# Kernel tuning notes

Measured on AMD Instinct MI355X. Metric: run time of the kernel, lower is better.

## Reference

```python
import jax, jax.numpy as jnp
import numpy as np

D, H, E, HID, TOPK = 1024, 16, 8, 2048, 2
B, L = 2, 2048

def setup_inputs() -> dict:
    key = jax.random.key(0)
    ks = jax.random.split(key, 12)
    s = 0.02
    return {
        "x": jax.random.normal(ks[0], (B, L, D), jnp.float32),
        "mask": jnp.zeros((B, L), dtype=bool),  # key_padding_mask: True = ignore
        "ln1_g": jnp.ones((D,), jnp.float32), "ln1_b": jnp.zeros((D,), jnp.float32),
        "Wqkv": jax.random.normal(ks[1], (3 * D, D), jnp.float32) * s,
        "bqkv": jnp.zeros((3 * D,), jnp.float32),
        "Wo": jax.random.normal(ks[2], (D, D), jnp.float32) * s,
        "bo": jnp.zeros((D,), jnp.float32),
        "ln2_g": jnp.ones((D,), jnp.float32), "ln2_b": jnp.zeros((D,), jnp.float32),
        "Wg": jax.random.normal(ks[3], (D, E), jnp.float32) * s,
        "bg": jnp.zeros((E,), jnp.float32),
        "W1": jax.random.normal(ks[4], (E, D, HID), jnp.float32) * s,
        "b1": jnp.zeros((E, HID), jnp.float32),
        "W2": jax.random.normal(ks[5], (E, HID, D), jnp.float32) * s,
        "b2": jnp.zeros((E, D), jnp.float32),
    }

def _layernorm(x, g, b, eps=1e-5):
    mu = x.mean(-1, keepdims=True)
    var = ((x - mu) ** 2).mean(-1, keepdims=True)
    return (x - mu) * jax.lax.rsqrt(var + eps) * g + b

def reference(x, mask, ln1_g, ln1_b, Wqkv, bqkv, Wo, bo, ln2_g, ln2_b, Wg, bg, W1, b1, W2, b2):
    b, l, d = x.shape
    dh = d // H
    # ---- pre-norm self-attention ----
    residual = x
    xn = _layernorm(x, ln1_g, ln1_b)
    qkv = xn @ Wqkv.T + bqkv                      # [B,L,3D]
    q, k, v = jnp.split(qkv, 3, axis=-1)
    q = q.reshape(b, l, H, dh).transpose(0, 2, 1, 3)  # bhld
    k = k.reshape(b, l, H, dh).transpose(0, 2, 1, 3)
    v = v.reshape(b, l, H, dh).transpose(0, 2, 1, 3)
    scores = jnp.einsum('bhqd,bhkd->bhqk', q, k) / jnp.sqrt(jnp.float32(dh))
    scores = jnp.where(mask[:, None, None, :], jnp.float32(-1e9), scores)
    attn = jax.nn.softmax(scores, axis=-1)
    ao = jnp.einsum('bhqk,bhkd->bhqd', attn, v).transpose(0, 2, 1, 3).reshape(b, l, d)
    ao = ao @ Wo.T + bo
    x = residual + ao                              # dropout is identity at eval
    # ---- pre-norm MoE FFN (top-2 softmax gating) ----
    residual = x
    xn = _layernorm(x, ln2_g, ln2_b)
    T = b * l
    xf = xn.reshape(T, d)
    probs = jax.nn.softmax(xf @ Wg + bg, axis=-1)  # [T,E]
    vals, idx = jax.lax.top_k(probs, TOPK)         # [T,K]
    wts = vals / vals.sum(-1, keepdims=True)
    # dense expert compute (reference): all experts over all tokens
    h = jax.nn.gelu(jnp.einsum('td,edh->eth', xf, W1) + b1[:, None, :], approximate=False)
    eo = jnp.einsum('eth,ehd->etd', h, W2) + b2[:, None, :]   # [E,T,D]
    sel = eo[idx, jnp.arange(T)[:, None]]          # [T,K,D]
    moe_out = (wts[..., None] * sel).sum(1).reshape(b, l, d)
    # load-balancing aux loss
    me = probs.mean(0)                             # mean gate prob per expert
    ce = jax.nn.one_hot(idx, E, dtype=probs.dtype).sum(1).mean(0)  # dispatch fraction
    moe_loss = jnp.float32(E) * jnp.sum(me * ce)
    out = residual + moe_out
    return (out, moe_loss)
```

## Files before the change

kernel.cpp:

```cpp
#include <hip/hip_runtime.h>
#include <stdint.h>

#define TOK   4096
#define DIM   1024
#define NH    16
#define DHD   64
#define NE    8
#define HIDN  2048
#define BATCH 2
#define SEQ   2048
#define BK    64

using floatx4 = __attribute__((ext_vector_type(4))) float;
using bfx8    = __attribute__((ext_vector_type(8))) __bf16;
using bfx2    = __attribute__((ext_vector_type(2))) __bf16;
using shortx8 = __attribute__((ext_vector_type(8))) short;

__device__ __forceinline__ unsigned short f2bf(float f) {
    union { __bf16 b; unsigned short u; } v;
    v.b = (__bf16)f;
    return v.u;
}

__device__ __forceinline__ unsigned pack2bf(float lo, float hi) {
    union { bfx2 v; unsigned u; } t;
    t.v[0] = (__bf16)lo;
    t.v[1] = (__bf16)hi;
    return t.u;
}

__device__ __forceinline__ floatx4 mfma16(bfx8 a, bfx8 b, floatx4 c) {
    return __builtin_amdgcn_mfma_f32_16x16x32_bf16(a, b, c, 0, 0, 0);
}

__device__ __forceinline__ void gload16(const unsigned short* g, unsigned short* l) {
    __builtin_amdgcn_global_load_lds(
        (const __attribute__((address_space(1))) unsigned int*)g,
        (__attribute__((address_space(3))) unsigned int*)l, 16, 0, 0);
}

__device__ __forceinline__ int xcd_swz(int hw, int nwg) {
    int q = nwg >> 3, r = nwg & 7;
    int xc = hw & 7, o = hw >> 3;
    return (xc < r ? xc * (q + 1) : r * (q + 1) + (xc - r) * q) + o;
}

__global__ __launch_bounds__(256) void cvt_kernel(const float* __restrict__ in,
                                                  unsigned short* __restrict__ out, int n) {
    int i = (blockIdx.x * 256 + threadIdx.x) * 4;
    if (i < n) {
        float4 v = *reinterpret_cast<const float4*>(in + i);
        out[i + 0] = f2bf(v.x);
        out[i + 1] = f2bf(v.y);
        out[i + 2] = f2bf(v.z);
        out[i + 3] = f2bf(v.w);
    }
}

__global__ __launch_bounds__(256) void transpose_cvt_kernel(const float* __restrict__ in,
                                                            unsigned short* __restrict__ out,
                                                            int R, int C) {
    __shared__ unsigned short t[64][65];
    in  += (size_t)blockIdx.z * R * C;
    out += (size_t)blockIdx.z * R * C;
    int r0 = blockIdx.y * 64, c0 = blockIdx.x * 64;
    int lr = threadIdx.x >> 4, lc = (threadIdx.x & 15) * 4;
#pragma unroll
    for (int p = 0; p < 4; p++) {
        int r = p * 16 + lr;
        float4 v = *reinterpret_cast<const float4*>(in + (size_t)(r0 + r) * C + c0 + lc);
        t[lc + 0][r] = f2bf(v.x);
        t[lc + 1][r] = f2bf(v.y);
        t[lc + 2][r] = f2bf(v.z);
        t[lc + 3][r] = f2bf(v.w);
    }
    __syncthreads();
    int c = threadIdx.x >> 2, ch = (threadIdx.x & 3) * 16;
    shortx8 o0, o1;
#pragma unroll
    for (int q = 0; q < 8; q++) { o0[q] = t[c][ch + q]; o1[q] = t[c][ch + 8 + q]; }
    unsigned short* op = out + (size_t)(c0 + c) * R + r0 + ch;
    *reinterpret_cast<shortx8*>(op) = o0;
    *reinterpret_cast<shortx8*>(op + 8) = o1;
}

__global__ __launch_bounds__(256) void kvprep_kernel(const unsigned short* __restrict__ qkv,
                                                     unsigned short* __restrict__ ktg,
                                                     unsigned short* __restrict__ vtg,
                                                     const unsigned char* __restrict__ mask,
                                                     float* __restrict__ maskf) {
    __shared__ unsigned short t[64 * 64];
    int tid = threadIdx.x;
    int s0 = blockIdx.x * 64, hd = blockIdx.y, b = blockIdx.z;
    size_t bh = (size_t)(b * NH + hd);
    if (hd == 0 && tid < 64) {
        maskf[(size_t)b * SEQ + s0 + tid] =
            mask[(size_t)b * SEQ + s0 + tid] ? -1.44269504e9f : 0.0f;
    }
#pragma unroll
    for (int i = 0; i < 2; i++) {
        int idx = i * 256 + tid;
        int sr = idx >> 3, c = idx & 7;
        shortx8 v = *reinterpret_cast<const shortx8*>(
            qkv + (size_t)(b * SEQ + s0 + sr) * 3 * DIM + DIM + hd * DHD + c * 8);
        *reinterpret_cast<shortx8*>(ktg + (bh * SEQ + s0 + sr) * DHD + c * 8) = v;
    }
#pragma unroll
    for (int i = 0; i < 2; i++) {
        int idx = i * 256 + tid;
        int sr = idx >> 3, c = idx & 7;
        shortx8 v = *reinterpret_cast<const shortx8*>(
            qkv + (size_t)(b * SEQ + s0 + sr) * 3 * DIM + 2 * DIM + hd * DHD + c * 8);
        *reinterpret_cast<shortx8*>(t + sr * 64 + ((c ^ (sr >> 3)) * 8)) = v;
    }
    __syncthreads();
#pragma unroll
    for (int i = 0; i < 2; i++) {
        int idx = i * 256 + tid;
        int d = idx >> 3, c2 = idx & 7;
        shortx8 o;
#pragma unroll
        for (int e = 0; e < 8; e++) {
            int s = c2 * 8 + e;
            o[e] = (short)t[s * 64 + (((d >> 3) ^ c2) * 8) + (d & 7)];
        }
        *reinterpret_cast<shortx8*>(vtg + (bh * DHD + d) * SEQ + s0 + c2 * 8) = o;
    }
}

__global__ __launch_bounds__(256) void ln_kernel(const float* __restrict__ x,
                                                 const float* __restrict__ g,
                                                 const float* __restrict__ b,
                                                 unsigned short* __restrict__ obf) {
    int t = blockIdx.x;
    int tid = threadIdx.x;
    const float* xr = x + (size_t)t * DIM;
    float4 v = *reinterpret_cast<const float4*>(xr + tid * 4);
    float s  = v.x + v.y + v.z + v.w;
    float s2 = v.x * v.x + v.y * v.y + v.z * v.z + v.w * v.w;
    for (int o = 32; o > 0; o >>= 1) {
        s  += __shfl_down(s,  o, 64);
        s2 += __shfl_down(s2, o, 64);
    }
    __shared__ float red[10];
    int lane = tid & 63, w = tid >> 6;
    if (lane == 0) { red[w] = s; red[4 + w] = s2; }
    __syncthreads();
    if (tid == 0) {
        float ts = red[0] + red[1] + red[2] + red[3];
        float t2 = red[4] + red[5] + red[6] + red[7];
        float mu = ts * (1.0f / DIM);
        float var = t2 * (1.0f / DIM) - mu * mu;
        red[8] = mu;
        red[9] = rsqrtf(var + 1e-5f);
    }
    __syncthreads();
    float mu = red[8], rstd = red[9];
    float4 gv = *reinterpret_cast<const float4*>(g + tid * 4);
    float4 bv = *reinterpret_cast<const float4*>(b + tid * 4);
    size_t o = (size_t)t * DIM + tid * 4;
    obf[o + 0] = f2bf((v.x - mu) * rstd * gv.x + bv.x);
    obf[o + 1] = f2bf((v.y - mu) * rstd * gv.y + bv.y);
    obf[o + 2] = f2bf((v.z - mu) * rstd * gv.z + bv.z);
    obf[o + 3] = f2bf((v.w - mu) * rstd * gv.w + bv.w);
}

template <int EPI, bool GATHER>
__global__ __launch_bounds__(256) void gemm_kernel(const unsigned short* __restrict__ A,
                                                   const unsigned short* __restrict__ Bt,
                                                   void* __restrict__ C,
                                                   const float* __restrict__ bias,
                                                   const float* __restrict__ resid,
                                                   const int* __restrict__ cnt,
                                                   const int* __restrict__ goff,
                                                   const int* __restrict__ gtok,
                                                   int M, int N, int K) {
    int gx = gridDim.x, gy = gridDim.y;
    int nwg = gx * gy * (int)gridDim.z;
    int hw = ((int)blockIdx.z * gy + (int)blockIdx.y) * gx + (int)blockIdx.x;
    int virt = xcd_swz(hw, nwg);
    int bx = virt % gx;
    int tmp = virt / gx;
    int by = tmp % gy;
    int e = tmp / gy;

    int Me = cnt ? cnt[e] : M;
    int brow = by * 128;
    if (brow >= Me) return;
    int bcol = bx * 128;
    int go = goff ? goff[e] : 0;
    const unsigned short* Be = Bt + (size_t)e * N * K;
    const float* biasp = bias + (size_t)e * N;

    __shared__ unsigned short As[128 * BK];
    __shared__ unsigned short Bs[128 * BK];

    int tid = threadIdx.x, lane = tid & 63, w = tid >> 6;
    int wr = w >> 1, wc = w & 1;
    int cg = lane >> 4, cl = lane & 15;

    const unsigned short* aga[4];
    const unsigned short* bga[4];
    unsigned short* asb = As + w * 2048;
    unsigned short* bsb = Bs + w * 2048;
#pragma unroll
    for (int i = 0; i < 4; i++) {
        int s = w * 256 + i * 64 + lane;
        int row = s >> 3;
        int c = (s & 7) ^ (row & 7);
        int gr = brow + row;
        if (gr >= Me) gr = Me - 1;
        long ar;
        if (GATHER) ar = gtok[go + gr];
        else if (cnt) ar = go + gr;
        else ar = gr;
        aga[i] = A + ar * (long)K + c * 8;
        bga[i] = Be + (size_t)(bcol + row) * K + c * 8;
    }

    floatx4 acc[4][4];
#pragma unroll
    for (int m = 0; m < 4; m++)
#pragma unroll
        for (int n = 0; n < 4; n++) acc[m][n] = (floatx4){0.f, 0.f, 0.f, 0.f};

    for (int kt = 0; kt < K; kt += BK) {
#pragma unroll
        for (int i = 0; i < 4; i++) {
            gload16(aga[i], asb + i * 512);
            gload16(bga[i], bsb + i * 512);
            aga[i] += BK;
            bga[i] += BK;
        }
        __syncthreads();
#pragma unroll
        for (int ks = 0; ks < 2; ks++) {
            bfx8 af[4], bf[4];
#pragma unroll
            for (int m = 0; m < 4; m++) {
                int row = wr * 64 + m * 16 + cl;
                af[m] = *reinterpret_cast<const bfx8*>(
                    As + row * BK + (((ks * 4 + cg) ^ (row & 7)) << 3));
            }
#pragma unroll
            for (int n = 0; n < 4; n++) {
                int row = wc * 64 + n * 16 + cl;
                bf[n] = *reinterpret_cast<const bfx8*>(
                    Bs + row * BK + (((ks * 4 + cg) ^ (row & 7)) << 3));
            }
#pragma unroll
            for (int m = 0; m < 4; m++)
#pragma unroll
                for (int n = 0; n < 4; n++) acc[m][n] = mfma16(af[m], bf[n], acc[m][n]);
        }
        __syncthreads();
    }

#pragma unroll
    for (int m = 0; m < 4; m++) {
#pragma unroll
        for (int j = 0; j < 4; j++) {
            int r = brow + wr * 64 + m * 16 + cg * 4 + j;
            if (r >= Me) continue;
#pragma unroll
            for (int n = 0; n < 4; n++) {
                int col = bcol + wc * 64 + n * 16 + cl;
                float v = acc[m][n][j] + biasp[col];
                if (EPI == 0) {
                    ((unsigned short*)C)[(size_t)r * N + col] = f2bf(v);
                } else if (EPI == 1) {
                    size_t o = (size_t)r * N + col;
                    ((float*)C)[o] = v + resid[o];
                } else if (EPI == 2) {
                    float gg = 0.5f * v * (1.0f + erff(v * 0.70710678f));
                    ((unsigned short*)C)[(size_t)(go + r) * N + col] = f2bf(gg);
                } else {
                    ((float*)C)[(size_t)(go + r) * N + col] = v;
                }
            }
        }
    }
}

__global__ __launch_bounds__(256, 2) void attn_kernel(const unsigned short* __restrict__ qkv,
                                                      const unsigned short* __restrict__ ktg,
                                                      const unsigned short* __restrict__ vtg,
                                                      const float* __restrict__ maskf,
                                                      unsigned short* __restrict__ ao) {
    __shared__ unsigned short Ks[2][64 * 64];
    __shared__ unsigned short Vs[2][64 * 64];
    __shared__ unsigned short Ps[4][2][16 * 72];

    int tid = threadIdx.x, lane = tid & 63, w = tid >> 6;
    int cg = lane >> 4, cl = lane & 15;
    int qb = blockIdx.x * 128, hd = blockIdx.y, b = blockIdx.z;
    size_t bh = (size_t)(b * NH + hd);
    const float SC2 = 0.125f * 1.44269504f;

    const unsigned short* qrow0 =
        qkv + (size_t)(b * SEQ + qb + w * 32 + cl) * 3 * DIM + hd * DHD;
    const unsigned short* qrow1 = qrow0 + (size_t)16 * 3 * DIM;
    bfx8 aq00 = *reinterpret_cast<const bfx8*>(qrow0 + cg * 8);
    bfx8 aq01 = *reinterpret_cast<const bfx8*>(qrow0 + 32 + cg * 8);
    bfx8 aq10 = *reinterpret_cast<const bfx8*>(qrow1 + cg * 8);
    bfx8 aq11 = *reinterpret_cast<const bfx8*>(qrow1 + 32 + cg * 8);

    int srow = lane >> 3, schunk = lane & 7;
    int sg = (schunk ^ srow) * 8;
    const unsigned short* kptr = ktg + (bh * SEQ + w * 16 + srow) * DHD + sg;
    const unsigned short* vptr = vtg + (bh * DHD + w * 16 + srow) * SEQ + sg;
    const float* mrowf = maskf + (size_t)b * SEQ;
    unsigned short* psw0 = &Ps[w][0][0];
    unsigned short* psw1 = &Ps[w][1][0];
    int sw0 = (cg ^ (cl & 7)) << 3;

    floatx4 accO0[4], accO1[4];
#pragma unroll
    for (int dt = 0; dt < 4; dt++) {
        accO0[dt] = (floatx4){0.f, 0.f, 0.f, 0.f};
        accO1[dt] = (floatx4){0.f, 0.f, 0.f, 0.f};
    }
    float m00 = -3.0e38f, l00 = 0.f;
    float m01 = -3.0e38f, l01 = 0.f;

    gload16(kptr, &Ks[0][w * 1024]);
    gload16(kptr + 8 * DHD, &Ks[0][w * 1024 + 512]);
    gload16(vptr, &Vs[0][w * 1024]);
    gload16(vptr + 8 * SEQ, &Vs[0][w * 1024 + 512]);
    __syncthreads();

    int cur = 0;
    for (int t = 0; t < SEQ / 64; t++) {
        if (t < SEQ / 64 - 1) {
            size_t nkt = (size_t)(t + 1) * 64;
            int nb = cur ^ 1;
            gload16(kptr + nkt * DHD, &Ks[nb][w * 1024]);
            gload16(kptr + nkt * DHD + 8 * DHD, &Ks[nb][w * 1024 + 512]);
            gload16(vptr + nkt, &Vs[nb][w * 1024]);
            gload16(vptr + nkt + 8 * SEQ, &Vs[nb][w * 1024 + 512]);
        }
        const unsigned short* ksb = &Ks[cur][0];
        const unsigned short* vsb = &Vs[cur][0];
        int kt = t * 64;

        floatx4 accS0[4], accS1[4];
#pragma unroll
        for (int nt = 0; nt < 4; nt++) {
            accS0[nt] = (floatx4){0.f, 0.f, 0.f, 0.f};
            accS1[nt] = (floatx4){0.f, 0.f, 0.f, 0.f};
        }
#pragma unroll
        for (int nt = 0; nt < 4; nt++) {
            const unsigned short* kr = ksb + (nt * 16 + cl) * 64;
            bfx8 k0 = *reinterpret_cast<const bfx8*>(kr + sw0);
            bfx8 k1 = *reinterpret_cast<const bfx8*>(kr + (sw0 ^ 32));
            accS0[nt] = mfma16(k0, aq00, accS0[nt]);
            accS0[nt] = mfma16(k1, aq01, accS0[nt]);
            accS1[nt] = mfma16(k0, aq10, accS1[nt]);
            accS1[nt] = mfma16(k1, aq11, accS1[nt]);
        }

        float4 mk[4];
#pragma unroll
        for (int nt = 0; nt < 4; nt++)
            mk[nt] = *reinterpret_cast<const float4*>(mrowf + kt + nt * 16 + cg * 4);

        {
            float s[4][4];
            float tmax = -3.0e38f;
#pragma unroll
            for (int nt = 0; nt < 4; nt++) {
                s[nt][0] = fmaf(accS0[nt][0], SC2, mk[nt].x);
                s[nt][1] = fmaf(accS0[nt][1], SC2, mk[nt].y);
                s[nt][2] = fmaf(accS0[nt][2], SC2, mk[nt].z);
                s[nt][3] = fmaf(accS0[nt][3], SC2, mk[nt].w);
#pragma unroll
                for (int j = 0; j < 4; j++) tmax = fmaxf(tmax, s[nt][j]);
            }
            if (!__all(tmax - m00 <= 11.5f)) {
                tmax = fmaxf(tmax, __shfl_xor(tmax, 16, 64));
                tmax = fmaxf(tmax, __shfl_xor(tmax, 32, 64));
                float mn = fmaxf(m00, tmax);
                float al = __builtin_amdgcn_exp2f(m00 - mn);
                m00 = mn;
                l00 *= al;
#pragma unroll
                for (int dt = 0; dt < 4; dt++) accO0[dt] *= al;
            }
            float rs = 0.f;
#pragma unroll
            for (int nt = 0; nt < 4; nt++) {
                float p0 = __builtin_amdgcn_exp2f(s[nt][0] - m00);
                float p1 = __builtin_amdgcn_exp2f(s[nt][1] - m00);
                float p2 = __builtin_amdgcn_exp2f(s[nt][2] - m00);
                float p3 = __builtin_amdgcn_exp2f(s[nt][3] - m00);
                rs += (p0 + p1) + (p2 + p3);
                uint2 u;
                u.x = pack2bf(p0, p1);
                u.y = pack2bf(p2, p3);
                *reinterpret_cast<uint2*>(psw0 + cl * 72 + nt * 16 + cg * 4) = u;
            }
            rs += __shfl_xor(rs, 16, 64);
            rs += __shfl_xor(rs, 32, 64);
            l00 += rs;
        }
        {
            float s[4][4];
            float tmax = -3.0e38f;
#pragma unroll
            for (int nt = 0; nt < 4; nt++) {
                s[nt][0] = fmaf(accS1[nt][0], SC2, mk[nt].x);
                s[nt][1] = fmaf(accS1[nt][1], SC2, mk[nt].y);
                s[nt][2] = fmaf(accS1[nt][2], SC2, mk[nt].z);
                s[nt][3] = fmaf(accS1[nt][3], SC2, mk[nt].w);
#pragma unroll
                for (int j = 0; j < 4; j++) tmax = fmaxf(tmax, s[nt][j]);
            }
            if (!__all(tmax - m01 <= 11.5f)) {
                tmax = fmaxf(tmax, __shfl_xor(tmax, 16, 64));
                tmax = fmaxf(tmax, __shfl_xor(tmax, 32, 64));
                float mn = fmaxf(m01, tmax);
                float al = __builtin_amdgcn_exp2f(m01 - mn);
                m01 = mn;
                l01 *= al;
#pragma unroll
                for (int dt = 0; dt < 4; dt++) accO1[dt] *= al;
            }
            float rs = 0.f;
#pragma unroll
            for (int nt = 0; nt < 4; nt++) {
                float p0 = __builtin_amdgcn_exp2f(s[nt][0] - m01);
                float p1 = __builtin_amdgcn_exp2f(s[nt][1] - m01);
                float p2 = __builtin_amdgcn_exp2f(s[nt][2] - m01);
                float p3 = __builtin_amdgcn_exp2f(s[nt][3] - m01);
                rs += (p0 + p1) + (p2 + p3);
                uint2 u;
                u.x = pack2bf(p0, p1);
                u.y = pack2bf(p2, p3);
                *reinterpret_cast<uint2*>(psw1 + cl * 72 + nt * 16 + cg * 4) = u;
            }
            rs += __shfl_xor(rs, 16, 64);
            rs += __shfl_xor(rs, 32, 64);
            l01 += rs;
        }

        bfx8 pf00 = *reinterpret_cast<const bfx8*>(psw0 + cl * 72 + cg * 8);
        bfx8 pf01 = *reinterpret_cast<const bfx8*>(psw0 + cl * 72 + 32 + cg * 8);
        bfx8 pf10 = *reinterpret_cast<const bfx8*>(psw1 + cl * 72 + cg * 8);
        bfx8 pf11 = *reinterpret_cast<const bfx8*>(psw1 + cl * 72 + 32 + cg * 8);
#pragma unroll
        for (int dt = 0; dt < 4; dt++) {
            const unsigned short* vr = vsb + (dt * 16 + cl) * 64;
            bfx8 v0 = *reinterpret_cast<const bfx8*>(vr + sw0);
            bfx8 v1 = *reinterpret_cast<const bfx8*>(vr + (sw0 ^ 32));
            accO0[dt] = mfma16(v0, pf00, accO0[dt]);
            accO0[dt] = mfma16(v1, pf01, accO0[dt]);
            accO1[dt] = mfma16(v0, pf10, accO1[dt]);
            accO1[dt] = mfma16(v1, pf11, accO1[dt]);
        }
        __syncthreads();
        cur ^= 1;
    }

    float rl0 = 1.0f / l00;
    float rl1 = 1.0f / l01;
    unsigned short* aorow0 =
        ao + (size_t)(b * SEQ + qb + w * 32 + cl) * DIM + hd * DHD;
    unsigned short* aorow1 = aorow0 + (size_t)16 * DIM;
#pragma unroll
    for (int dt = 0; dt < 4; dt++) {
        uint2 u;
        u.x = pack2bf(accO0[dt][0] * rl0, accO0[dt][1] * rl0);
        u.y = pack2bf(accO0[dt][2] * rl0, accO0[dt][3] * rl0);
        *reinterpret_cast<uint2*>(aorow0 + dt * 16 + cg * 4) = u;
        u.x = pack2bf(accO1[dt][0] * rl1, accO1[dt][1] * rl1);
        u.y = pack2bf(accO1[dt][2] * rl1, accO1[dt][3] * rl1);
        *reinterpret_cast<uint2*>(aorow1 + dt * 16 + cg * 4) = u;
    }
}

__global__ __launch_bounds__(256) void gate_kernel(const float* __restrict__ x2,
                                                   const float* __restrict__ lng,
                                                   const float* __restrict__ lnb,
                                                   const float* __restrict__ Wg,
                                                   const float* __restrict__ bg,
                                                   unsigned short* __restrict__ xn2b,
                                                   int* __restrict__ idx,
                                                   float* __restrict__ wts,
                                                   float* __restrict__ me_part) {
    __shared__ float bme[8];
    if (threadIdx.x < 8) bme[threadIdx.x] = 0.f;
    __syncthreads();
    int w = threadIdx.x >> 6, lane = threadIdx.x & 63;
    int t = blockIdx.x * 4 + w;
    const float* xr = x2 + (size_t)t * DIM + lane * 16;
    float4 xv[4];
    float s = 0.f, s2 = 0.f;
#pragma unroll
    for (int q = 0; q < 4; q++) {
        xv[q] = *reinterpret_cast<const float4*>(xr + q * 4);
        s  += xv[q].x + xv[q].y + xv[q].z + xv[q].w;
        s2 += xv[q].x * xv[q].x + xv[q].y * xv[q].y + xv[q].z * xv[q].z + xv[q].w * xv[q].w;
    }
    for (int o = 32; o > 0; o >>= 1) {
        s  += __shfl_xor(s,  o, 64);
        s2 += __shfl_xor(s2, o, 64);
    }
    float mu = s * (1.0f / DIM);
    float rstd = rsqrtf(s2 * (1.0f / DIM) - mu * mu + 1e-5f);
    float acc[8];
#pragma unroll
    for (int e = 0; e < 8; e++) acc[e] = 0.f;
    unsigned short ob[16];
#pragma unroll
    for (int q = 0; q < 4; q++) {
        float4 gv = *reinterpret_cast<const float4*>(lng + lane * 16 + q * 4);
        float4 bv = *reinterpret_cast<const float4*>(lnb + lane * 16 + q * 4);
        float xn0 = (xv[q].x - mu) * rstd * gv.x + bv.x;
        float xn1 = (xv[q].y - mu) * rstd * gv.y + bv.y;
        float xn2 = (xv[q].z - mu) * rstd * gv.z + bv.z;
        float xn3 = (xv[q].w - mu) * rstd * gv.w + bv.w;
        ob[q * 4 + 0] = f2bf(xn0);
        ob[q * 4 + 1] = f2bf(xn1);
        ob[q * 4 + 2] = f2bf(xn2);
        ob[q * 4 + 3] = f2bf(xn3);
        const float* wr = Wg + (size_t)(lane * 16 + q * 4) * 8;
#pragma unroll
        for (int e = 0; e < 8; e++) acc[e] += xn0 * wr[e];
#pragma unroll
        for (int e = 0; e < 8; e++) acc[e] += xn1 * wr[8 + e];
#pragma unroll
        for (int e = 0; e < 8; e++) acc[e] += xn2 * wr[16 + e];
#pragma unroll
        for (int e = 0; e < 8; e++) acc[e] += xn3 * wr[24 + e];
    }
    unsigned short* op = xn2b + (size_t)t * DIM + lane * 16;
    *reinterpret_cast<shortx8*>(op)     = *reinterpret_cast<shortx8*>(&ob[0]);
    *reinterpret_cast<shortx8*>(op + 8) = *reinterpret_cast<shortx8*>(&ob[8]);
    for (int o = 32; o > 0; o >>= 1)
#pragma unroll
        for (int e = 0; e < 8; e++) acc[e] += __shfl_xor(acc[e], o, 64);
    if (lane == 0) {
        float p[8];
        float mx = -3e38f;
#pragma unroll
        for (int e = 0; e < 8; e++) { acc[e] += bg[e]; mx = fmaxf(mx, acc[e]); }
        float se = 0.f;
#pragma unroll
        for (int e = 0; e < 8; e++) { p[e] = expf(acc[e] - mx); se += p[e]; }
#pragma unroll
        for (int e = 0; e < 8; e++) p[e] /= se;
        int i0 = 0; float v0 = p[0];
#pragma unroll
        for (int e = 1; e < 8; e++) if (p[e] > v0) { v0 = p[e]; i0 = e; }
        int i1 = -1; float v1 = -3e38f;
#pragma unroll
        for (int e = 0; e < 8; e++) if (e != i0 && p[e] > v1) { v1 = p[e]; i1 = e; }
        float sw = v0 + v1;
        idx[t * 2]     = i0;
        idx[t * 2 + 1] = i1;
        wts[t * 2]     = v0 / sw;
        wts[t * 2 + 1] = v1 / sw;
#pragma unroll
        for (int e = 0; e < 8; e++) atomicAdd(&bme[e], p[e]);
    }
    __syncthreads();
    if (threadIdx.x < 8) me_part[(size_t)blockIdx.x * 8 + threadIdx.x] = bme[threadIdx.x];
}

__global__ __launch_bounds__(256) void route1_kernel(const int* __restrict__ idx,
                                                     int* __restrict__ cnt,
                                                     int* __restrict__ posl) {
    __shared__ int lh[8];
    __shared__ int gb[8];
    int tid = threadIdx.x;
    int t = blockIdx.x * 256 + tid;
    if (tid < 8) lh[tid] = 0;
    __syncthreads();
    int i0 = idx[t * 2], i1 = idx[t * 2 + 1];
    int r0 = atomicAdd(&lh[i0], 1);
    int r1 = atomicAdd(&lh[i1], 1);
    __syncthreads();
    if (tid < 8) gb[tid] = atomicAdd(&cnt[tid], lh[tid]);
    __syncthreads();
    posl[t * 2]     = gb[i0] + r0;
    posl[t * 2 + 1] = gb[i1] + r1;
}

__global__ void prefix_kernel(const int* __restrict__ cnt, int* __restrict__ goff) {
    if (threadIdx.x == 0) {
        int s = 0;
        for (int e = 0; e < 8; e++) { goff[e] = s; s += cnt[e]; }
        goff[8] = s;
    }
}

__global__ __launch_bounds__(256) void route2_kernel(const int* __restrict__ idx,
                                                     const int* __restrict__ goff,
                                                     const int* __restrict__ posl,
                                                     int* __restrict__ gtok,
                                                     int* __restrict__ tpos) {
    int t = blockIdx.x * 256 + threadIdx.x;
#pragma unroll
    for (int j = 0; j < 2; j++) {
        int e = idx[t * 2 + j];
        int p = goff[e] + posl[t * 2 + j];
        gtok[p] = t;
        tpos[t * 2 + j] = p;
    }
}

__global__ __launch_bounds__(256) void combine_kernel(const float* __restrict__ x2,
                                                      const float* __restrict__ eo,
                                                      const float* __restrict__ wts,
                                                      const int* __restrict__ tpos,
                                                      float* __restrict__ out) {
    int t = blockIdx.x;
    int c = threadIdx.x * 4;
    float w0 = wts[t * 2], w1 = wts[t * 2 + 1];
    int p0 = tpos[t * 2], p1 = tpos[t * 2 + 1];
    float4 r  = *reinterpret_cast<const float4*>(x2 + (size_t)t * DIM + c);
    float4 a  = *reinterpret_cast<const float4*>(eo + (size_t)p0 * DIM + c);
    float4 bb = *reinterpret_cast<const float4*>(eo + (size_t)p1 * DIM + c);
    float4 o;
    o.x = r.x + w0 * a.x + w1 * bb.x;
    o.y = r.y + w0 * a.y + w1 * bb.y;
    o.z = r.z + w0 * a.z + w1 * bb.z;
    o.w = r.w + w0 * a.w + w1 * bb.w;
    *reinterpret_cast<float4*>(out + (size_t)t * DIM + c) = o;
}

__global__ __launch_bounds__(256) void loss_kernel(const float* __restrict__ me_part,
                                                   const int* __restrict__ cnt,
                                                   float* __restrict__ out) {
    __shared__ float red[256];
    int tid = threadIdx.x;
    int e = tid & 7, part = tid >> 3;
    float s = 0.f;
    for (int b = part; b < 1024; b += 32) s += me_part[(size_t)b * 8 + e];
    red[tid] = s;
    __syncthreads();
    if (tid < 64) {
        float v = red[tid] + red[tid + 64] + red[tid + 128] + red[tid + 192];
        red[tid] = v;
    }
    __syncthreads();
    if (tid < 8) {
        float v = red[tid] + red[tid + 8] + red[tid + 16] + red[tid + 24] +
                  red[tid + 32] + red[tid + 40] + red[tid + 48] + red[tid + 56];
        red[tid] = v;
    }
    __syncthreads();
    if (tid == 0) {
        float s2 = 0.f;
        for (int ee = 0; ee < 8; ee++)
            s2 += (red[ee] / 4096.0f) * ((float)cnt[ee] / 4096.0f);
        out[(size_t)TOK * DIM] = 8.0f * s2;
    }
}

extern "C" void kernel_launch(void* const* d_in, const int* in_sizes, int n_in,
                              void* d_out, int out_size, void* d_ws, size_t ws_size,
                              hipStream_t stream) {
    const float* x    = (const float*)d_in[0];
    const unsigned char* mask = (const unsigned char*)d_in[1];
    const float* ln1g = (const float*)d_in[2];
    const float* ln1b = (const float*)d_in[3];
    const float* Wqkv = (const float*)d_in[4];
    const float* bqkv = (const float*)d_in[5];
    const float* Wo   = (const float*)d_in[6];
    const float* bo   = (const float*)d_in[7];
    const float* ln2g = (const float*)d_in[8];
    const float* ln2b = (const float*)d_in[9];
    const float* Wg   = (const float*)d_in[10];
    const float* bg   = (const float*)d_in[11];
    const float* W1   = (const float*)d_in[12];
    const float* b1   = (const float*)d_in[13];
    const float* W2   = (const float*)d_in[14];
    const float* b2   = (const float*)d_in[15];
    float* out = (float*)d_out;

    char* ws = (char*)d_ws;
    int*   cnt  = (int*)(ws + 0);
    int*   goff = (int*)(ws + 128);
    size_t off = 1024;
    auto alloc = [&](size_t bytes) -> void* {
        void* p = ws + off;
        off += (bytes + 255) & ~(size_t)255;
        return p;
    };
    const size_t SZ_QKVB = (size_t)TOK * 3 * DIM * 2;
    const size_t SZ_HB   = (size_t)2 * TOK * HIDN * 2;
    const size_t SZ_EOF  = (size_t)2 * TOK * DIM * 4;
    char* R1 = (char*)alloc(SZ_HB > SZ_QKVB ? SZ_HB : SZ_QKVB);
    char* R2 = (char*)alloc(SZ_EOF);
    unsigned short* qkvb  = (unsigned short*)R1;
    unsigned short* hb    = (unsigned short*)R1;
    float*          eof   = (float*)R2;
    unsigned short* xn1   = (unsigned short*)R2;
    unsigned short* aob   = (unsigned short*)(R2 + (size_t)TOK * DIM * 2);
    unsigned short* wqkvb = (unsigned short*)(R2 + (size_t)2 * TOK * DIM * 2);
    unsigned short* wob   = (unsigned short*)(R2 + (size_t)2 * TOK * DIM * 2 +
                                              (size_t)3 * DIM * DIM * 2);
    float*          x2    = (float*)alloc((size_t)TOK * DIM * 4);
    unsigned short* xn2b  = (unsigned short*)alloc((size_t)TOK * DIM * 2);
    unsigned short* w1t   = (unsigned short*)alloc((size_t)NE * DIM * HIDN * 2);
    unsigned short* w2t   = (unsigned short*)alloc((size_t)NE * DIM * HIDN * 2);
    unsigned short* ktg   = (unsigned short*)alloc((size_t)BATCH * NH * SEQ * DHD * 2);
    unsigned short* vtg   = (unsigned short*)alloc((size_t)BATCH * NH * DHD * SEQ * 2);
    float*          maskf = (float*)alloc((size_t)BATCH * SEQ * 4);
    float*          mep   = (float*)alloc((size_t)1024 * 8 * 4);
    int*            idxp  = (int*)alloc((size_t)TOK * 2 * 4);
    float*          wtsp  = (float*)alloc((size_t)TOK * 2 * 4);
    int*            posl  = (int*)alloc((size_t)TOK * 2 * 4);
    int*            gtok  = (int*)alloc((size_t)2 * TOK * 4);
    int*            tpos  = (int*)alloc((size_t)TOK * 2 * 4);

    hipMemsetAsync(ws, 0, 256, stream);

    cvt_kernel<<<3 * DIM * DIM / 1024, 256, 0, stream>>>(Wqkv, wqkvb, 3 * DIM * DIM);
    cvt_kernel<<<DIM * DIM / 1024, 256, 0, stream>>>(Wo, wob, DIM * DIM);
    transpose_cvt_kernel<<<dim3(HIDN / 64, DIM / 64, NE), 256, 0, stream>>>(W1, w1t, DIM, HIDN);
    transpose_cvt_kernel<<<dim3(DIM / 64, HIDN / 64, NE), 256, 0, stream>>>(W2, w2t, HIDN, DIM);

    ln_kernel<<<TOK, 256, 0, stream>>>(x, ln1g, ln1b, xn1);

    gemm_kernel<0, false><<<dim3(24, 32, 1), 256, 0, stream>>>(
        xn1, wqkvb, qkvb, bqkv, nullptr, nullptr, nullptr, nullptr, TOK, 3 * DIM, DIM);

    kvprep_kernel<<<dim3(SEQ / 64, NH, BATCH), 256, 0, stream>>>(qkvb, ktg, vtg, mask, maskf);

    attn_kernel<<<dim3(SEQ / 128, NH, BATCH), 256, 0, stream>>>(qkvb, ktg, vtg, maskf, aob);

    gemm_kernel<1, false><<<dim3(8, 32, 1), 256, 0, stream>>>(
        aob, wob, x2, bo, x, nullptr, nullptr, nullptr, TOK, DIM, DIM);

    gate_kernel<<<TOK / 4, 256, 0, stream>>>(x2, ln2g, ln2b, Wg, bg, xn2b,
                                             idxp, wtsp, mep);
    route1_kernel<<<TOK / 256, 256, 0, stream>>>(idxp, cnt, posl);
    prefix_kernel<<<1, 64, 0, stream>>>(cnt, goff);
    route2_kernel<<<TOK / 256, 256, 0, stream>>>(idxp, goff, posl, gtok, tpos);

    gemm_kernel<2, true><<<dim3(16, 32, 8), 256, 0, stream>>>(
        xn2b, w1t, hb, b1, nullptr, cnt, goff, gtok, TOK, HIDN, DIM);

    gemm_kernel<3, false><<<dim3(8, 32, 8), 256, 0, stream>>>(
        hb, w2t, eof, b2, nullptr, cnt, goff, nullptr, TOK, DIM, HIDN);

    combine_kernel<<<TOK, 256, 0, stream>>>(x2, eof, wtsp, tpos, out);
    loss_kernel<<<1, 256, 0, stream>>>(mep, cnt, out);
}
```

Baseline: 366.6 us.

## Double-buffer GEMM LDS tiles and store expert outputs in bf16

The shared GEMM kernel now uses two LDS buffers, so it prefetches the next K tile with global_load_lds while computing on the current one, and the second sync per iteration no longer waits on an exposed load. Separately, the second expert GEMM writes its outputs as bf16 instead of fp32, and the combine kernel reads bf16 and converts. This halves the traffic for the expert-output intermediate. It doubles GEMM LDS use to 64KB per block, which can lower occupancy, and adds bf16 rounding error on the expert outputs.

```diff
diff --git a/kernel.cpp b/kernel.cpp
--- a/kernel.cpp
+++ b/kernel.cpp
@@ -20,6 +20,12 @@
     union { __bf16 b; unsigned short u; } v;
     v.b = (__bf16)f;
     return v.u;
+}
+
+__device__ __forceinline__ float bf2f(unsigned short u) {
+    union { unsigned u; float f; } v;
+    v.u = (unsigned)u << 16;
+    return v.f;
 }
 
 __device__ __forceinline__ unsigned pack2bf(float lo, float hi) {
@@ -192,8 +198,8 @@
     const unsigned short* Be = Bt + (size_t)e * N * K;
     const float* biasp = bias + (size_t)e * N;
 
-    __shared__ unsigned short As[128 * BK];
-    __shared__ unsigned short Bs[128 * BK];
+    __shared__ unsigned short As[2 * 128 * BK];
+    __shared__ unsigned short Bs[2 * 128 * BK];
 
     int tid = threadIdx.x, lane = tid & 63, w = tid >> 6;
     int wr = w >> 1, wc = w & 1;
@@ -201,8 +207,6 @@
 
     const unsigned short* aga[4];
     const unsigned short* bga[4];
-    unsigned short* asb = As + w * 2048;
-    unsigned short* bsb = Bs + w * 2048;
 #pragma unroll
     for (int i = 0; i < 4; i++) {
         int s = w * 256 + i * 64 + lane;
@@ -224,15 +228,30 @@
 #pragma unroll
         for (int n = 0; n < 4; n++) acc[m][n] = (floatx4){0.f, 0.f, 0.f, 0.f};
 
-    for (int kt = 0; kt < K; kt += BK) {
-#pragma unroll
-        for (int i = 0; i < 4; i++) {
-            gload16(aga[i], asb + i * 512);
-            gload16(bga[i], bsb + i * 512);
-            aga[i] += BK;
-            bga[i] += BK;
-        }
-        __syncthreads();
+#pragma unroll
+    for (int i = 0; i < 4; i++) {
+        gload16(aga[i], As + w * 2048 + i * 512);
+        gload16(bga[i], Bs + w * 2048 + i * 512);
+        aga[i] += BK;
+        bga[i] += BK;
+    }
+    __syncthreads();
+
+    int nt = K / BK;
+    int cur = 0;
+    for (int t = 0; t < nt; t++) {
+        if (t + 1 < nt) {
+            int nb = cur ^ 1;
+#pragma unroll
+            for (int i = 0; i < 4; i++) {
+                gload16(aga[i], As + nb * 8192 + w * 2048 + i * 512);
+                gload16(bga[i], Bs + nb * 8192 + w * 2048 + i * 512);
+                aga[i] += BK;
+                bga[i] += BK;
+            }
+        }
+        const unsigned short* asb = As + cur * 8192;
+        const unsigned short* bsb = Bs + cur * 8192;
 #pragma unroll
         for (int ks = 0; ks < 2; ks++) {
             bfx8 af[4], bf[4];
@@ -240,13 +259,13 @@
             for (int m = 0; m < 4; m++) {
                 int row = wr * 64 + m * 16 + cl;
                 af[m] = *reinterpret_cast<const bfx8*>(
-                    As + row * BK + (((ks * 4 + cg) ^ (row & 7)) << 3));
+                    asb + row * BK + (((ks * 4 + cg) ^ (row & 7)) << 3));
             }
 #pragma unroll
             for (int n = 0; n < 4; n++) {
                 int row = wc * 64 + n * 16 + cl;
                 bf[n] = *reinterpret_cast<const bfx8*>(
-                    Bs + row * BK + (((ks * 4 + cg) ^ (row & 7)) << 3));
+                    bsb + row * BK + (((ks * 4 + cg) ^ (row & 7)) << 3));
             }
 #pragma unroll
             for (int m = 0; m < 4; m++)
@@ -254,6 +273,7 @@
                 for (int n = 0; n < 4; n++) acc[m][n] = mfma16(af[m], bf[n], acc[m][n]);
         }
         __syncthreads();
+        cur ^= 1;
     }
 
 #pragma unroll
@@ -275,7 +295,7 @@
                     float gg = 0.5f * v * (1.0f + erff(v * 0.70710678f));
                     ((unsigned short*)C)[(size_t)(go + r) * N + col] = f2bf(gg);
                 } else {
-                    ((float*)C)[(size_t)(go + r) * N + col] = v;
+                    ((unsigned short*)C)[(size_t)(go + r) * N + col] = f2bf(v);
                 }
             }
         }
@@ -611,7 +631,7 @@
 }
 
 __global__ __launch_bounds__(256) void combine_kernel(const float* __restrict__ x2,
-                                                      const float* __restrict__ eo,
+                                                      const unsigned short* __restrict__ eo,
                                                       const float* __restrict__ wts,
                                                       const int* __restrict__ tpos,
                                                       float* __restrict__ out) {
@@ -619,14 +639,14 @@
     int c = threadIdx.x * 4;
     float w0 = wts[t * 2], w1 = wts[t * 2 + 1];
     int p0 = tpos[t * 2], p1 = tpos[t * 2 + 1];
-    float4 r  = *reinterpret_cast<const float4*>(x2 + (size_t)t * DIM + c);
-    float4 a  = *reinterpret_cast<const float4*>(eo + (size_t)p0 * DIM + c);
-    float4 bb = *reinterpret_cast<const float4*>(eo + (size_t)p1 * DIM + c);
+    float4 r = *reinterpret_cast<const float4*>(x2 + (size_t)t * DIM + c);
+    ushort4 a4 = *reinterpret_cast<const ushort4*>(eo + (size_t)p0 * DIM + c);
+    ushort4 b4 = *reinterpret_cast<const ushort4*>(eo + (size_t)p1 * DIM + c);
     float4 o;
-    o.x = r.x + w0 * a.x + w1 * bb.x;
-    o.y = r.y + w0 * a.y + w1 * bb.y;
-    o.z = r.z + w0 * a.z + w1 * bb.z;
-    o.w = r.w + w0 * a.w + w1 * bb.w;
+    o.x = r.x + w0 * bf2f(a4.x) + w1 * bf2f(b4.x);
+    o.y = r.y + w0 * bf2f(a4.y) + w1 * bf2f(b4.y);
+    o.z = r.z + w0 * bf2f(a4.z) + w1 * bf2f(b4.z);
+    o.w = r.w + w0 * bf2f(a4.w) + w1 * bf2f(b4.w);
     *reinterpret_cast<float4*>(out + (size_t)t * DIM + c) = o;
 }
 
@@ -691,12 +711,13 @@
     };
     const size_t SZ_QKVB = (size_t)TOK * 3 * DIM * 2;
     const size_t SZ_HB   = (size_t)2 * TOK * HIDN * 2;
-    const size_t SZ_EOF  = (size_t)2 * TOK * DIM * 4;
     char* R1 = (char*)alloc(SZ_HB > SZ_QKVB ? SZ_HB : SZ_QKVB);
-    char* R2 = (char*)alloc(SZ_EOF);
+    const size_t SZ_R2 = (size_t)2 * TOK * DIM * 2 + (size_t)3 * DIM * DIM * 2 +
+                         (size_t)DIM * DIM * 2;
+    char* R2 = (char*)alloc(SZ_R2);
     unsigned short* qkvb  = (unsigned short*)R1;
     unsigned short* hb    = (unsigned short*)R1;
-    float*          eof   = (float*)R2;
+    unsigned short* eo16  = (unsigned short*)R2;
     unsigned short* xn1   = (unsigned short*)R2;
     unsigned short* aob   = (unsigned short*)(R2 + (size_t)TOK * DIM * 2);
     unsigned short* wqkvb = (unsigned short*)(R2 + (size_t)2 * TOK * DIM * 2);
@@ -745,8 +766,8 @@
         xn2b, w1t, hb, b1, nullptr, cnt, goff, gtok, TOK, HIDN, DIM);
 
     gemm_kernel<3, false><<<dim3(8, 32, 8), 256, 0, stream>>>(
-        hb, w2t, eof, b2, nullptr, cnt, goff, nullptr, TOK, DIM, HIDN);
-
-    combine_kernel<<<TOK, 256, 0, stream>>>(x2, eof, wtsp, tpos, out);
+        hb, w2t, eo16, b2, nullptr, cnt, goff, nullptr, TOK, DIM, HIDN);
+
+    combine_kernel<<<TOK, 256, 0, stream>>>(x2, eo16, wtsp, tpos, out);
     loss_kernel<<<1, 256, 0, stream>>>(mep, cnt, out);
 }
```

New measurement: 404.3 us. 10.3% more time.
